# Kernel optimization log

Measured on AMD Instinct MI355X. Metric: run time of the kernel, lower is better.

Reference implementation:

```python
import jax, jax.numpy as jnp
import numpy as np

C = 1024
H = 16
EPS = 1e-5

def _layernorm(x, g, b):
    mu = jnp.mean(x, axis=-1, keepdims=True)
    var = jnp.mean(jnp.square(x - mu), axis=-1, keepdims=True)
    return (x - mu) * jax.lax.rsqrt(var + EPS) * g + b

def _mha(xq, xkv, wq, bq, wk, bk, wv, bv, wo, bo, causal):
    B, T, Cm = xq.shape
    Tc = xkv.shape[1]
    d = Cm // H
    q = (xq @ wq + bq).reshape(B, T, H, d)
    k = (xkv @ wk + bk).reshape(B, Tc, H, d)
    v = (xkv @ wv + bv).reshape(B, Tc, H, d)
    att = jnp.einsum('bthd,bshd->bhts', q, k) * (1.0 / np.sqrt(d))
    if causal:
        mask = jnp.tril(jnp.ones((T, Tc), dtype=bool))
        att = jnp.where(mask[None, None], att, -jnp.inf)
    att = jax.nn.softmax(att, axis=-1)
    y = jnp.einsum('bhts,bshd->bthd', att, v).reshape(B, T, Cm)
    return y @ wo + bo


def setup_inputs() -> dict:
    key = jax.random.key(0)
    ks = jax.random.split(key, 20)
    s = 0.02
    w = lambda k: (s * jax.random.normal(k, (C, C))).astype(jnp.float32)
    inp = {
        'x': jax.random.normal(ks[0], (4, 1024, C), dtype=jnp.float32),
        'context': jax.random.normal(ks[1], (4, 1024, C), dtype=jnp.float32),
        'ln1_g': jnp.ones((C,)), 'ln1_b': jnp.zeros((C,)),
        'ln2_g': jnp.ones((C,)), 'ln2_b': jnp.zeros((C,)),
        'sa_wq': w(ks[2]), 'sa_bq': jnp.zeros((C,)),
        'sa_wk': w(ks[3]), 'sa_bk': jnp.zeros((C,)),
        'sa_wv': w(ks[4]), 'sa_bv': jnp.zeros((C,)),
        'sa_wo': w(ks[5]), 'sa_bo': jnp.zeros((C,)),
        'ca_wq': w(ks[6]), 'ca_bq': jnp.zeros((C,)),
        'ca_wk': w(ks[7]), 'ca_bk': jnp.zeros((C,)),
        'ca_wv': w(ks[8]), 'ca_bv': jnp.zeros((C,)),
        'ca_wo': w(ks[9]), 'ca_bo': jnp.zeros((C,)),
        'mlp_w1': (s * jax.random.normal(ks[10], (C, 4 * C))).astype(jnp.float32),
        'mlp_b1': jnp.zeros((4 * C,)),
        'mlp_w2': (s * jax.random.normal(ks[11], (4 * C, C))).astype(jnp.float32),
        'mlp_b2': jnp.zeros((C,)),
    }
    return inp


def reference(x, context, ln1_g, ln1_b, ln2_g, ln2_b,
              sa_wq, sa_bq, sa_wk, sa_bk, sa_wv, sa_bv, sa_wo, sa_bo,
              ca_wq, ca_bq, ca_wk, ca_bk, ca_wv, ca_bv, ca_wo, ca_bo,
              mlp_w1, mlp_b1, mlp_w2, mlp_b2):
    # x = x + self_attn(ln1(x))  (causal)
    x = x + _mha(_layernorm(x, ln1_g, ln1_b), _layernorm(x, ln1_g, ln1_b),
                 sa_wq, sa_bq, sa_wk, sa_bk, sa_wv, sa_bv, sa_wo, sa_bo, causal=True)
    # x = x + cross_attn(ln2(x), context)  (non-causal)
    x = x + _mha(_layernorm(x, ln2_g, ln2_b), context,
                 ca_wq, ca_bq, ca_wk, ca_bk, ca_wv, ca_bv, ca_wo, ca_bo, causal=False)
    # x = x + mlp(ln2(x))  -- note: the module reuses ln2 here (as in source)
    h = _layernorm(x, ln2_g, ln2_b)
    h = jax.nn.gelu(h @ mlp_w1 + mlp_b1, approximate=False) @ mlp_w2 + mlp_b2
    x = x + h
    return x
```

## Files before the change

### kernel.cpp

```cpp
#include <hip/hip_runtime.h>
#include <hip/hip_bf16.h>

typedef __attribute__((ext_vector_type(8))) short s8v;
typedef __attribute__((ext_vector_type(4))) float f4v;

#define DEV static __device__ __forceinline__

DEV unsigned short f2bf(float f) {
    unsigned int u = __builtin_bit_cast(unsigned int, f);
    unsigned int r = u + 0x7FFFu + ((u >> 16) & 1u);
    return (unsigned short)(r >> 16);
}

DEV f4v fzero() { f4v v = {0.f, 0.f, 0.f, 0.f}; return v; }

DEV float fgelu(float x) {
    float z = x * (1.5957691f + 0.07135482f * x * x);
    float s = __builtin_amdgcn_rcpf(1.0f + __expf(-z));
    return x * s;
}

DEV void gload16(const void* g, void* l) {
    __builtin_amdgcn_global_load_lds(
        (const __attribute__((address_space(1))) unsigned int*)g,
        (__attribute__((address_space(3))) unsigned int*)l, 16, 0, 0);
}

struct P8 { const float* p[8]; };
__global__ __launch_bounds__(256) void k_transpose8(
        P8 ws8, unsigned short* __restrict__ base) {
    __shared__ float tile[32][33];
    int z = blockIdx.z;
    const float* W = ws8.p[z];
    unsigned short* Wt = base + (size_t)z * 1024 * 1024;
    int tx = threadIdx.x & 31, ty = threadIdx.x >> 5;
    int n0 = blockIdx.x * 32, k0 = blockIdx.y * 32;
#pragma unroll
    for (int r = 0; r < 32; r += 8)
        tile[ty + r][tx] = W[(size_t)(k0 + ty + r) * 1024 + n0 + tx];
    __syncthreads();
#pragma unroll
    for (int r = 0; r < 32; r += 8)
        Wt[(size_t)(n0 + ty + r) * 1024 + k0 + tx] = f2bf(tile[tx][ty + r]);
}

__global__ __launch_bounds__(256) void k_transpose_bf16(
        const float* __restrict__ W, unsigned short* __restrict__ Wt, int K, int N) {
    __shared__ float tile[32][33];
    int tx = threadIdx.x & 31, ty = threadIdx.x >> 5;
    int n0 = blockIdx.x * 32, k0 = blockIdx.y * 32;
#pragma unroll
    for (int r = 0; r < 32; r += 8)
        tile[ty + r][tx] = W[(size_t)(k0 + ty + r) * N + n0 + tx];
    __syncthreads();
#pragma unroll
    for (int r = 0; r < 32; r += 8)
        Wt[(size_t)(n0 + ty + r) * K + k0 + tx] = f2bf(tile[tx][ty + r]);
}

__global__ __launch_bounds__(256) void k_f32_to_bf16(
        const float* __restrict__ in, unsigned short* __restrict__ out, int n) {
    int i = (blockIdx.x * 256 + threadIdx.x) * 8;
    if (i >= n) return;
    float4 a = *(const float4*)(in + i);
    float4 b = *(const float4*)(in + i + 4);
    uint4 o;
    o.x = f2bf(a.x) | ((unsigned)f2bf(a.y) << 16);
    o.y = f2bf(a.z) | ((unsigned)f2bf(a.w) << 16);
    o.z = f2bf(b.x) | ((unsigned)f2bf(b.y) << 16);
    o.w = f2bf(b.z) | ((unsigned)f2bf(b.w) << 16);
    *(uint4*)(out + i) = o;
}

__global__ __launch_bounds__(256) void k_bias_cat(
        const float* q, const float* k, const float* v,
        const float* k2, const float* v2, float* out) {
    int i = blockIdx.x * 256 + threadIdx.x;
    float val;
    if (i < 1024) val = q[i];
    else if (i < 2048) val = k[i - 1024];
    else if (i < 3072) val = v[i - 2048];
    else if (i < 4096) val = k2[i - 3072];
    else val = v2[i - 4096];
    out[i] = val;
}

__global__ __launch_bounds__(256) void k_layernorm(
        const float* __restrict__ x, const float* __restrict__ g,
        const float* __restrict__ b, unsigned short* __restrict__ out) {
    int row = blockIdx.x;
    int t = threadIdx.x;
    const float* xr = x + (size_t)row * 1024;
    float4 v = *(const float4*)(xr + t * 4);
    float s = v.x + v.y + v.z + v.w;
    float ss = v.x * v.x + v.y * v.y + v.z * v.z + v.w * v.w;
#pragma unroll
    for (int m = 1; m < 64; m <<= 1) { s += __shfl_xor(s, m); ss += __shfl_xor(ss, m); }
    __shared__ float red[16];
    int w = t >> 6;
    if ((t & 63) == 0) { red[w] = s; red[8 + w] = ss; }
    __syncthreads();
    s = red[0] + red[1] + red[2] + red[3];
    ss = red[8] + red[9] + red[10] + red[11];
    float mu = s * (1.f / 1024.f);
    float rstd = rsqrtf(ss * (1.f / 1024.f) - mu * mu + 1e-5f);
    float4 gv = *(const float4*)(g + t * 4);
    float4 bv = *(const float4*)(b + t * 4);
    float y0 = (v.x - mu) * rstd * gv.x + bv.x;
    float y1 = (v.y - mu) * rstd * gv.y + bv.y;
    float y2 = (v.z - mu) * rstd * gv.z + bv.z;
    float y3 = (v.w - mu) * rstd * gv.w + bv.w;
    uint2 o;
    o.x = f2bf(y0) | ((unsigned)f2bf(y1) << 16);
    o.y = f2bf(y2) | ((unsigned)f2bf(y3) << 16);
    *(uint2*)(out + (size_t)row * 1024 + t * 4) = o;
}

template <int EPI, int BM>
__global__ __launch_bounds__(256) void k_gemm(
        const unsigned short* __restrict__ A, const unsigned short* __restrict__ Bt,
        const float* __restrict__ bias, const float* __restrict__ res,
        void* __restrict__ outv, int M, int N, int K) {
    constexpr int WI = (BM == 128) ? 4 : 2;
    constexpr int ABUF = BM * 64;
    constexpr int BUFSZ = ABUF + 8192;
    __shared__ __align__(16) char smem[3 * BUFSZ];
    int nbx = N >> 7;
    int bid = blockIdx.x;
    int cpx = gridDim.x >> 3;
    int swz = (bid & 7) * cpx + (bid >> 3);
    int bx = swz % nbx, by = swz / nbx;
    int m0 = by * BM, n0 = bx << 7;
    int tid = threadIdx.x, w = tid >> 6, l = tid & 63;
    int wr = w >> 1, wc = w & 1;
    int lq = l >> 4, lc = l & 15;
    f4v acc[WI][4];
#pragma unroll
    for (int i = 0; i < WI; ++i)
#pragma unroll
        for (int j = 0; j < 4; ++j) acc[i][j] = fzero();
    const unsigned short* Ab = A + (size_t)m0 * K;
    const unsigned short* Bb = Bt + (size_t)n0 * K;
    int arow = w * 16 + (l >> 2);
    int ach = (((l & 3) ^ ((arow >> 1) & 3)) << 3);

    auto STAGE = [&](int t) {
        int kt = t << 5;
        char* buf = smem + (t % 3) * BUFSZ;
        gload16(Ab + (size_t)arow * K + kt + ach, buf + w * 1024);
        if constexpr (BM == 128)
            gload16(Ab + (size_t)(64 + arow) * K + kt + ach, buf + 4096 + w * 1024);
        gload16(Bb + (size_t)arow * K + kt + ach, buf + ABUF + w * 1024);
        gload16(Bb + (size_t)(64 + arow) * K + kt + ach, buf + ABUF + 4096 + w * 1024);
    };
    int cs = ((lq ^ ((lc >> 1) & 3)) << 4);
    auto COMPUTE = [&](int t) {
        const char* buf = smem + (t % 3) * BUFSZ;
        s8v af[WI], bfr[4];
#pragma unroll
        for (int i = 0; i < WI; ++i)
            af[i] = *(const s8v*)(buf + (wr * (BM / 2) + i * 16 + lc) * 64 + cs);
#pragma unroll
        for (int j = 0; j < 4; ++j)
            bfr[j] = *(const s8v*)(buf + ABUF + (wc * 64 + j * 16 + lc) * 64 + cs);
#pragma unroll
        for (int i = 0; i < WI; ++i)
#pragma unroll
            for (int j = 0; j < 4; ++j)
                acc[i][j] = __builtin_amdgcn_mfma_f32_16x16x32_bf16(af[i], bfr[j], acc[i][j], 0, 0, 0);
    };

    int NT = K >> 5;
    STAGE(0); STAGE(1);
    if constexpr (BM == 128) asm volatile("s_waitcnt vmcnt(4)" ::: "memory");
    else                     asm volatile("s_waitcnt vmcnt(3)" ::: "memory");
    __builtin_amdgcn_s_barrier();
    for (int t = 0; t < NT; ++t) {
        if (t + 2 < NT) STAGE(t + 2);
        COMPUTE(t);
        if (t + 2 < NT) {
            if constexpr (BM == 128) asm volatile("s_waitcnt vmcnt(4)" ::: "memory");
            else                     asm volatile("s_waitcnt vmcnt(3)" ::: "memory");
        } else if (t + 1 < NT) {
            asm volatile("s_waitcnt vmcnt(0)" ::: "memory");
        }
        __builtin_amdgcn_s_barrier();
    }

    float* esc = (float*)smem + w * 1088;
#pragma unroll
    for (int i = 0; i < WI; ++i) {
#pragma unroll
        for (int j = 0; j < 4; ++j)
#pragma unroll
            for (int r = 0; r < 4; ++r)
                esc[(lq * 4 + r) * 68 + j * 16 + lc] = acc[i][j][r];
#pragma unroll
        for (int p = 0; p < 4; ++p) {
            int rr = p * 4 + lq;
            float4 v = *(const float4*)(esc + rr * 68 + lc * 4);
            int row = m0 + wr * (BM / 2) + i * 16 + rr;
            int col = n0 + wc * 64 + lc * 4;
            float4 bv = *(const float4*)(bias + col);
            v.x += bv.x; v.y += bv.y; v.z += bv.z; v.w += bv.w;
            size_t idx = (size_t)row * N + col;
            if (EPI == 0) {
                ushort4 o;
                o.x = f2bf(v.x); o.y = f2bf(v.y); o.z = f2bf(v.z); o.w = f2bf(v.w);
                *(ushort4*)((unsigned short*)outv + idx) = o;
            } else if (EPI == 1) {
                ushort4 o;
                o.x = f2bf(fgelu(v.x)); o.y = f2bf(fgelu(v.y));
                o.z = f2bf(fgelu(v.z)); o.w = f2bf(fgelu(v.w));
                *(ushort4*)((unsigned short*)outv + idx) = o;
            } else {
                float4 rv = *(const float4*)(res + idx);
                v.x += rv.x; v.y += rv.y; v.z += rv.z; v.w += rv.w;
                *(float4*)((float*)outv + idx) = v;
            }
        }
    }
}

template <bool CAUSAL>
__global__ __launch_bounds__(256) void k_attn(
        const unsigned short* __restrict__ Q, int ldq,
        const unsigned short* __restrict__ Kp, int ldk,
        const unsigned short* __restrict__ Vp, int ldv,
        unsigned short* __restrict__ O, int ldo, int T) {
    __shared__ unsigned short Ks[2][64 * 64];
    __shared__ unsigned short Vt[2][64 * 64];
    __shared__ unsigned short Ps[4][16 * 64];
    int nqt = T >> 6;
    int qt0, qt1, bh;
    if (CAUSAL) {
        int pairs = nqt >> 1;
        int pr = blockIdx.x % pairs;
        bh = blockIdx.x / pairs;
        qt0 = pr; qt1 = nqt - 1 - pr;
    } else {
        qt1 = blockIdx.x % nqt;
        bh = blockIdx.x / nqt;
        qt0 = 0;
    }
    int b = bh >> 4, h = bh & 15;
    int tid = threadIdx.x, w = tid >> 6, l = tid & 63;
    int lq = l >> 4, lc = l & 15;
    size_t qoff = (size_t)b * T * ldq + h * 64;
    size_t koff = (size_t)b * T * ldk + h * 64;
    size_t voff = (size_t)b * T * ldv + h * 64;
    s8v qf1[2], qf0[2];
    {
        const unsigned short* qp = Q + qoff + (size_t)(qt1 * 64 + w * 16 + lc) * ldq + lq * 8;
        qf1[0] = *(const s8v*)qp;
        qf1[1] = *(const s8v*)(qp + 32);
        if (CAUSAL) {
            const unsigned short* q0p = Q + qoff + (size_t)(qt0 * 64 + w * 16 + lc) * ldq + lq * 8;
            qf0[0] = *(const s8v*)q0p;
            qf0[1] = *(const s8v*)(q0p + 32);
        }
    }
    s8v ones;
#pragma unroll
    for (int i = 0; i < 8; ++i) ones[i] = (short)0x3F80;
    f4v o1[4], o0[4];
    float l1r[4], l0r[4];
    float m1 = -3.0e38f, m0 = -3.0e38f;
#pragma unroll
    for (int j = 0; j < 4; ++j) {
        o1[j] = fzero(); o0[j] = fzero(); l1r[j] = 0.f; l0r[j] = 0.f;
    }
    int p = tid & 31, dbase = (tid >> 5) * 8;
    s8v v0r, v1r;

    auto STAGE_K = [&](int kt, int bufi) {
#pragma unroll
        for (int s = 0; s < 2; ++s) {
            int idx = s * 256 + w * 64 + l;
            int t = idx >> 3;
            int ch = (idx & 7) ^ (t & 7);
            gload16(Kp + koff + (size_t)(kt * 64 + t) * ldk + ch * 8,
                    (char*)Ks[bufi] + s * 4096 + w * 1024);
        }
    };
    auto LOAD_V = [&](int kt) {
        const unsigned short* vp = Vp + voff + (size_t)(kt * 64 + 2 * p) * ldv + dbase;
        v0r = *(const s8v*)vp;
        v1r = *(const s8v*)(vp + ldv);
    };
    auto WRITE_V = [&](int bufi) {
#pragma unroll
        for (int j = 0; j < 8; ++j) {
            int dd = dbase + j;
            unsigned int val = (unsigned short)v0r[j] | ((unsigned)(unsigned short)v1r[j] << 16);
            *(unsigned int*)((char*)Vt[bufi] + dd * 128 +
                             ((((p >> 2) ^ (dd & 7)) << 4) | ((p & 3) << 2))) = val;
        }
    };

    const float SC = 0.18033688011112042f;

    auto SMPV = [&](f4v (&sa)[4], f4v (&oa)[4], float& mr, float (&lr)[4],
                    int bufi, int qt, int kt) {
        bool diag = CAUSAL && (kt == qt);
        int qloc = w * 16 + lc;
        float pv[16];
        float tm = -3.0e38f;
#pragma unroll
        for (int jn = 0; jn < 4; ++jn)
#pragma unroll
            for (int j = 0; j < 4; ++j) {
                float sv = sa[jn][j] * SC;
                if (diag && (jn * 16 + lq * 4 + j > qloc)) sv = -3.0e38f;
                pv[jn * 4 + j] = sv;
                tm = fmaxf(tm, sv);
            }
        tm = fmaxf(tm, __shfl_xor(tm, 16));
        tm = fmaxf(tm, __shfl_xor(tm, 32));
        float mnew = fmaxf(mr, tm);
        float alpha = exp2f(mr - mnew);
        mr = mnew;
#pragma unroll
        for (int j = 0; j < 4; ++j) {
            float aj = __shfl(alpha, lq * 4 + j);
            lr[j] *= aj;
#pragma unroll
            for (int jn = 0; jn < 4; ++jn) oa[jn][j] *= aj;
        }
#pragma unroll
        for (int jn = 0; jn < 4; ++jn) {
            int chunk = (jn * 2 + (lq >> 1)) ^ (lc & 7);
            char* basep = (char*)Ps[w] + lc * 128 + (chunk << 4) + ((lq & 1) << 3);
            unsigned e01 = f2bf(exp2f(pv[jn * 4 + 0] - mnew)) |
                           ((unsigned)f2bf(exp2f(pv[jn * 4 + 1] - mnew)) << 16);
            unsigned e23 = f2bf(exp2f(pv[jn * 4 + 2] - mnew)) |
                           ((unsigned)f2bf(exp2f(pv[jn * 4 + 3] - mnew)) << 16);
            *(unsigned*)basep = e01;
            *(unsigned*)(basep + 4) = e23;
        }
        s8v pa[2];
#pragma unroll
        for (int kc = 0; kc < 2; ++kc)
            pa[kc] = *(const s8v*)((const char*)Ps[w] + lc * 128 +
                                   (((kc * 4 + lq) ^ (lc & 7)) << 4));
        f4v sone = fzero();
#pragma unroll
        for (int kc = 0; kc < 2; ++kc) {
            sone = __builtin_amdgcn_mfma_f32_16x16x32_bf16(pa[kc], ones, sone, 0, 0, 0);
#pragma unroll
            for (int jn = 0; jn < 4; ++jn) {
                int dd = jn * 16 + lc;
                s8v bf = *(const s8v*)((const char*)Vt[bufi] + dd * 128 +
                                       (((kc * 4 + lq) ^ (dd & 7)) << 4));
                oa[jn] = __builtin_amdgcn_mfma_f32_16x16x32_bf16(pa[kc], bf, oa[jn], 0, 0, 0);
            }
        }
#pragma unroll
        for (int j = 0; j < 4; ++j) lr[j] += sone[j];
    };

    int ktend = CAUSAL ? (qt1 + 1) : nqt;
    STAGE_K(0, 0); LOAD_V(0);
    asm volatile("s_waitcnt vmcnt(0)" ::: "memory");
    WRITE_V(0);
    __syncthreads();
    int buf = 0;
    for (int kt = 0; kt < ktend; ++kt) {
        bool pf = (kt + 1 < ktend);
        if (pf) { STAGE_K(kt + 1, buf ^ 1); LOAD_V(kt + 1); }
        bool do0 = CAUSAL && (kt <= qt0);
        f4v sa1[4], sa0[4];
#pragma unroll
        for (int jn = 0; jn < 4; ++jn) {
            sa1[jn] = fzero(); sa0[jn] = fzero();
            int t = jn * 16 + lc;
#pragma unroll
            for (int kc = 0; kc < 2; ++kc) {
                s8v kf = *(const s8v*)((const char*)Ks[buf] + t * 128 +
                                       (((kc * 4 + lq) ^ (t & 7)) << 4));
                sa1[jn] = __builtin_amdgcn_mfma_f32_16x16x32_bf16(kf, qf1[kc], sa1[jn], 0, 0, 0);
                if (do0)
                    sa0[jn] = __builtin_amdgcn_mfma_f32_16x16x32_bf16(kf, qf0[kc], sa0[jn], 0, 0, 0);
            }
        }
        SMPV(sa1, o1, m1, l1r, buf, qt1, kt);
        if (do0) SMPV(sa0, o0, m0, l0r, buf, qt0, kt);
        if (pf) {
            asm volatile("s_waitcnt vmcnt(0)" ::: "memory");
            WRITE_V(buf ^ 1);
        }
        __syncthreads();
        buf ^= 1;
    }
#pragma unroll
    for (int j = 0; j < 4; ++j) {
        float inv = 1.0f / l1r[j];
        int row = qt1 * 64 + w * 16 + lq * 4 + j;
#pragma unroll
        for (int jn = 0; jn < 4; ++jn)
            O[(size_t)(b * T + row) * ldo + h * 64 + jn * 16 + lc] = f2bf(o1[jn][j] * inv);
    }
    if (CAUSAL) {
#pragma unroll
        for (int j = 0; j < 4; ++j) {
            float inv = 1.0f / l0r[j];
            int row = qt0 * 64 + w * 16 + lq * 4 + j;
#pragma unroll
            for (int jn = 0; jn < 4; ++jn)
                O[(size_t)(b * T + row) * ldo + h * 64 + jn * 16 + lc] = f2bf(o0[jn][j] * inv);
        }
    }
}

extern "C" void kernel_launch(void* const* d_in, const int* in_sizes, int n_in,
                              void* d_out, int out_size, void* d_ws, size_t ws_size,
                              hipStream_t stream) {
    const float* x     = (const float*)d_in[0];
    const float* ctx   = (const float*)d_in[1];
    const float* ln1_g = (const float*)d_in[2];
    const float* ln1_b = (const float*)d_in[3];
    const float* ln2_g = (const float*)d_in[4];
    const float* ln2_b = (const float*)d_in[5];
    const float* sa_wq = (const float*)d_in[6];  const float* sa_bq = (const float*)d_in[7];
    const float* sa_wk = (const float*)d_in[8];  const float* sa_bk = (const float*)d_in[9];
    const float* sa_wv = (const float*)d_in[10]; const float* sa_bv = (const float*)d_in[11];
    const float* sa_wo = (const float*)d_in[12]; const float* sa_bo = (const float*)d_in[13];
    const float* ca_wq = (const float*)d_in[14]; const float* ca_bq = (const float*)d_in[15];
    const float* ca_wk = (const float*)d_in[16]; const float* ca_bk = (const float*)d_in[17];
    const float* ca_wv = (const float*)d_in[18]; const float* ca_bv = (const float*)d_in[19];
    const float* ca_wo = (const float*)d_in[20]; const float* ca_bo = (const float*)d_in[21];
    const float* w1 = (const float*)d_in[22]; const float* b1 = (const float*)d_in[23];
    const float* w2 = (const float*)d_in[24]; const float* b2 = (const float*)d_in[25];
    float* out = (float*)d_out;

    char* ws = (char*)d_ws;
    const size_t MB = 1024 * 1024;
    unsigned short* wt_base = (unsigned short*)(ws + 0 * MB);
    unsigned short* wt_saq = wt_base + 0 * 1024 * 1024;
    unsigned short* wt_cak = wt_base + 5 * 1024 * 1024;
    unsigned short* wt_sao = wt_base + 3 * 1024 * 1024;
    unsigned short* wt_caq = wt_base + 4 * 1024 * 1024;
    unsigned short* wt_cao = wt_base + 7 * 1024 * 1024;
    unsigned short* w1t    = (unsigned short*)(ws + 16 * MB);
    unsigned short* w2t    = (unsigned short*)(ws + 24 * MB);
    unsigned short* ctxb   = (unsigned short*)(ws + 32 * MB);
    float*          x1     = (float*)        (ws + 40 * MB);
    unsigned short* qbuf   = (unsigned short*)(ws + 56 * MB);
    unsigned short* kbuf   = (unsigned short*)(ws + 64 * MB);
    unsigned short* hln    = (unsigned short*)(ws + 80 * MB);
    float*          bcat   = (float*)        (ws + 88 * MB);
    unsigned short* qkv = qbuf;
    unsigned short* kv  = kbuf;
    unsigned short* m1  = qbuf;
    unsigned short* h3  = ctxb;

    dim3 blk(256);
    P8 ws8;
    ws8.p[0] = sa_wq; ws8.p[1] = sa_wk; ws8.p[2] = sa_wv; ws8.p[3] = sa_wo;
    ws8.p[4] = ca_wq; ws8.p[5] = ca_wk; ws8.p[6] = ca_wv; ws8.p[7] = ca_wo;
    k_transpose8<<<dim3(32, 32, 8), blk, 0, stream>>>(ws8, wt_base);
    k_transpose_bf16<<<dim3(128, 32), blk, 0, stream>>>(w1, w1t, 1024, 4096);
    k_transpose_bf16<<<dim3(32, 128), blk, 0, stream>>>(w2, w2t, 4096, 1024);
    k_f32_to_bf16<<<dim3(2048), blk, 0, stream>>>(ctx, ctxb, 4 * 1024 * 1024);
    k_bias_cat<<<dim3(20), blk, 0, stream>>>(sa_bq, sa_bk, sa_bv, ca_bk, ca_bv, bcat);

    k_layernorm<<<dim3(4096), blk, 0, stream>>>(x, ln1_g, ln1_b, hln);
    k_gemm<0, 128><<<dim3(24 * 32), blk, 0, stream>>>(hln, wt_saq, bcat, nullptr, qkv, 4096, 3072, 1024);
    k_attn<true><<<dim3(512), blk, 0, stream>>>(qkv, 3072, qkv + 1024, 3072, qkv + 2048, 3072,
                                                hln, 1024, 1024);
    k_gemm<2, 64><<<dim3(64 * 8), blk, 0, stream>>>(hln, wt_sao, sa_bo, x, x1, 4096, 1024, 1024);

    k_layernorm<<<dim3(4096), blk, 0, stream>>>(x1, ln2_g, ln2_b, hln);
    k_gemm<0, 64><<<dim3(64 * 8), blk, 0, stream>>>(hln, wt_caq, ca_bq, nullptr, qbuf, 4096, 1024, 1024);
    k_gemm<0, 128><<<dim3(16 * 32), blk, 0, stream>>>(ctxb, wt_cak, bcat + 3072, nullptr, kv, 4096, 2048, 1024);
    k_attn<false><<<dim3(1024), blk, 0, stream>>>(qbuf, 1024, kv, 2048, kv + 1024, 2048,
                                                  hln, 1024, 1024);
    k_gemm<2, 64><<<dim3(64 * 8), blk, 0, stream>>>(hln, wt_cao, ca_bo, x1, out, 4096, 1024, 1024);

    k_layernorm<<<dim3(4096), blk, 0, stream>>>(out, ln2_g, ln2_b, h3);
    k_gemm<1, 128><<<dim3(32 * 32), blk, 0, stream>>>(h3, w1t, b1, nullptr, m1, 4096, 4096, 1024);
    k_gemm<2, 64><<<dim3(64 * 8), blk, 0, stream>>>(m1, w2t, b2, out, out, 4096, 1024, 4096);
}
```

Measured before the change: 352.8 us.

## Add 128x256-tile triple-buffered GEMM for QKV and MLP up-projection

Result: no change. 347.9 us (-1.4%).

```diff
diff --git a/kernel.cpp b/kernel.cpp
--- a/kernel.cpp
+++ b/kernel.cpp
@@ -222,6 +222,106 @@
     }
 }
 
+template <int EPI>
+__global__ __launch_bounds__(256, 2) void k_gemm2(
+        const unsigned short* __restrict__ A, const unsigned short* __restrict__ Bt,
+        const float* __restrict__ bias, void* __restrict__ outv,
+        int M, int N, int K) {
+    constexpr int BUFSZ = 8192 + 16384;
+    __shared__ __align__(16) char smem[3 * BUFSZ];
+    int nbx = N >> 8;
+    int bid = blockIdx.x;
+    int cpx = gridDim.x >> 3;
+    int swz = (bid & 7) * cpx + (bid >> 3);
+    int bx = swz % nbx, by = swz / nbx;
+    int m0 = by << 7, n0 = bx << 8;
+    int tid = threadIdx.x, w = tid >> 6, l = tid & 63;
+    int wr = w >> 1, wc = w & 1;
+    int lq = l >> 4, lc = l & 15;
+    f4v acc[4][8];
+#pragma unroll
+    for (int i = 0; i < 4; ++i)
+#pragma unroll
+        for (int j = 0; j < 8; ++j) acc[i][j] = fzero();
+    const unsigned short* Ab = A + (size_t)m0 * K;
+    const unsigned short* Bb = Bt + (size_t)n0 * K;
+    int arow = w * 16 + (l >> 2);
+    int ach = (((l & 3) ^ ((arow >> 1) & 3)) << 3);
+
+    auto STAGE = [&](int t) {
+        int kt = t << 5;
+        char* buf = smem + (t % 3) * BUFSZ;
+        gload16(Ab + (size_t)arow * K + kt + ach, buf + w * 1024);
+        gload16(Ab + (size_t)(64 + arow) * K + kt + ach, buf + 4096 + w * 1024);
+#pragma unroll
+        for (int h = 0; h < 4; ++h)
+            gload16(Bb + (size_t)(h * 64 + arow) * K + kt + ach,
+                    buf + 8192 + h * 4096 + w * 1024);
+    };
+    int cs = ((lq ^ ((lc >> 1) & 3)) << 4);
+    auto COMPUTE = [&](int t) {
+        const char* buf = smem + (t % 3) * BUFSZ;
+        s8v af[4], bfr[8];
+#pragma unroll
+        for (int i = 0; i < 4; ++i)
+            af[i] = *(const s8v*)(buf + (wr * 64 + i * 16 + lc) * 64 + cs);
+#pragma unroll
+        for (int j = 0; j < 8; ++j)
+            bfr[j] = *(const s8v*)(buf + 8192 + (wc * 128 + j * 16 + lc) * 64 + cs);
+#pragma unroll
+        for (int i = 0; i < 4; ++i)
+#pragma unroll
+            for (int j = 0; j < 8; ++j)
+                acc[i][j] = __builtin_amdgcn_mfma_f32_16x16x32_bf16(af[i], bfr[j], acc[i][j], 0, 0, 0);
+    };
+
+    int NT = K >> 5;
+    STAGE(0); STAGE(1);
+    asm volatile("s_waitcnt vmcnt(6)" ::: "memory");
+    __builtin_amdgcn_s_barrier();
+    for (int t = 0; t < NT; ++t) {
+        if (t + 2 < NT) STAGE(t + 2);
+        COMPUTE(t);
+        if (t + 2 < NT) {
+            asm volatile("s_waitcnt vmcnt(6)" ::: "memory");
+        } else if (t + 1 < NT) {
+            asm volatile("s_waitcnt vmcnt(0)" ::: "memory");
+        }
+        __builtin_amdgcn_s_barrier();
+    }
+
+    float* esc = (float*)smem + w * 2112;
+#pragma unroll
+    for (int i = 0; i < 4; ++i) {
+#pragma unroll
+        for (int j = 0; j < 8; ++j)
+#pragma unroll
+            for (int r = 0; r < 4; ++r)
+                esc[(lq * 4 + r) * 132 + j * 16 + lc] = acc[i][j][r];
+#pragma unroll
+        for (int p = 0; p < 4; ++p) {
+            int rr = p * 4 + lq;
+            int row = m0 + wr * 64 + i * 16 + rr;
+#pragma unroll
+            for (int h = 0; h < 2; ++h) {
+                float4 v = *(const float4*)(esc + rr * 132 + h * 64 + lc * 4);
+                int col = n0 + wc * 128 + h * 64 + lc * 4;
+                float4 bv = *(const float4*)(bias + col);
+                v.x += bv.x; v.y += bv.y; v.z += bv.z; v.w += bv.w;
+                size_t idx = (size_t)row * N + col;
+                ushort4 o;
+                if (EPI == 0) {
+                    o.x = f2bf(v.x); o.y = f2bf(v.y); o.z = f2bf(v.z); o.w = f2bf(v.w);
+                } else {
+                    o.x = f2bf(fgelu(v.x)); o.y = f2bf(fgelu(v.y));
+                    o.z = f2bf(fgelu(v.z)); o.w = f2bf(fgelu(v.w));
+                }
+                *(ushort4*)((unsigned short*)outv + idx) = o;
+            }
+        }
+    }
+}
+
 template <bool CAUSAL>
 __global__ __launch_bounds__(256) void k_attn(
         const unsigned short* __restrict__ Q, int ldq,
@@ -465,7 +565,7 @@
     k_bias_cat<<<dim3(20), blk, 0, stream>>>(sa_bq, sa_bk, sa_bv, ca_bk, ca_bv, bcat);
 
     k_layernorm<<<dim3(4096), blk, 0, stream>>>(x, ln1_g, ln1_b, hln);
-    k_gemm<0, 128><<<dim3(24 * 32), blk, 0, stream>>>(hln, wt_saq, bcat, nullptr, qkv, 4096, 3072, 1024);
+    k_gemm2<0><<<dim3(32 * 12), blk, 0, stream>>>(hln, wt_saq, bcat, qkv, 4096, 3072, 1024);
     k_attn<true><<<dim3(512), blk, 0, stream>>>(qkv, 3072, qkv + 1024, 3072, qkv + 2048, 3072,
                                                 hln, 1024, 1024);
     k_gemm<2, 64><<<dim3(64 * 8), blk, 0, stream>>>(hln, wt_sao, sa_bo, x, x1, 4096, 1024, 1024);
@@ -478,6 +578,6 @@
     k_gemm<2, 64><<<dim3(64 * 8), blk, 0, stream>>>(hln, wt_cao, ca_bo, x1, out, 4096, 1024, 1024);
 
     k_layernorm<<<dim3(4096), blk, 0, stream>>>(out, ln2_g, ln2_b, h3);
-    k_gemm<1, 128><<<dim3(32 * 32), blk, 0, stream>>>(h3, w1t, b1, nullptr, m1, 4096, 4096, 1024);
+    k_gemm2<1><<<dim3(32 * 16), blk, 0, stream>>>(h3, w1t, b1, m1, 4096, 4096, 1024);
     k_gemm<2, 64><<<dim3(64 * 8), blk, 0, stream>>>(m1, w2t, b2, out, out, 4096, 1024, 4096);
 }
```
